# Kernel tuning notes

Measured on AMD Instinct MI355X. Metric: run time of the kernel, lower is better.

Reference implementation:

```python
import jax, jax.numpy as jnp
import numpy as np

M, N, D = 512, 4096, 128
H = N // D  # 32
L = 4096   # cache length


def setup_inputs() -> dict:
    key = jax.random.key(0)
    ks = jax.random.split(key, 6)
    s = 1.0 / np.sqrt(N)
    return {
        "X": jax.random.normal(ks[0], (M, N), jnp.float32),
        "W_q": jax.random.normal(ks[1], (N, N), jnp.float32) * s,
        "W_k": jax.random.normal(ks[2], (N, N), jnp.float32) * s,
        "W_v": jax.random.normal(ks[3], (N, N), jnp.float32) * s,
        "cache_K": jax.random.normal(ks[4], (H, L, D), jnp.float32),
        "cache_V": jax.random.normal(ks[5], (H, L, D), jnp.float32),
        "P": 3584,
    }


def reference(X, W_q, W_k, W_v, cache_K, cache_V, P):
    # nn.Linear(N, N, bias=False): y = x @ W.T
    q = (X @ W_q.T).reshape(M, H, D).transpose(1, 0, 2)  # [H, M, D]
    k = (X @ W_k.T).reshape(M, H, D).transpose(1, 0, 2)  # [H, M, D]
    v = (X @ W_v.T).reshape(M, H, D).transpose(1, 0, 2)  # [H, M, D]
    # KV-cache write at position P (static slice under jit for fixed P)
    cK = jax.lax.dynamic_update_slice(cache_K, k, (0, P, 0))  # [H, L, D]
    cV = jax.lax.dynamic_update_slice(cache_V, v, (0, P, 0))
    # attention over the full cache, no 1/sqrt(D) scaling (faithful to source)
    scores = jnp.einsum("hmd,hld->hml", q, cK)   # [H, M, L]
    weights = jax.nn.softmax(scores, axis=-1)
    out = jnp.einsum("hml,hld->hmd", weights, cV)  # [H, M, D]
    return out.transpose(1, 0, 2).reshape(M, H * D)  # [M, N]
```

## Files before the change

kernel.cpp:

```cpp
#include <hip/hip_runtime.h>
#include <hip/hip_fp16.h>

typedef _Float16 f16x8 __attribute__((ext_vector_type(8)));
typedef float    f32x4 __attribute__((ext_vector_type(4)));

#define MFMA16(a,b,c) __builtin_amdgcn_mfma_f32_16x16x32_f16(a,b,c,0,0,0)

__device__ __forceinline__ void gload_lds16(const void* g, void* l) {
  __builtin_amdgcn_global_load_lds(
      (const __attribute__((address_space(1))) void*)g,
      (__attribute__((address_space(3))) void*)l, 16, 0, 0);
}

__global__ void cvt_f32_f16(const float* __restrict__ src,
                            _Float16* __restrict__ dst, int n8) {
  int i = blockIdx.x * blockDim.x + threadIdx.x;
  int stride = gridDim.x * blockDim.x;
  for (; i < n8; i += stride) {
    const float4* s = (const float4*)src + 2 * (size_t)i;
    float4 a = s[0], b = s[1];
    f16x8 o;
    o[0]=(_Float16)a.x; o[1]=(_Float16)a.y; o[2]=(_Float16)a.z; o[3]=(_Float16)a.w;
    o[4]=(_Float16)b.x; o[5]=(_Float16)b.y; o[6]=(_Float16)b.z; o[7]=(_Float16)b.w;
    ((f16x8*)dst)[i] = o;
  }
}

__global__ __launch_bounds__(256) void qkv_gemm_fused(
    const _Float16* __restrict__ X,
    const float* __restrict__ Wq,
    const float* __restrict__ Wk,
    const float* __restrict__ Wv,
    const float* __restrict__ cK,
    const float* __restrict__ cV,
    _Float16* __restrict__ Q16,
    _Float16* __restrict__ Kc,
    _Float16* __restrict__ Vt16,
    const int* __restrict__ Pp)
{
  __shared__ __align__(16) _Float16 As[128 * 64];
  __shared__ __align__(16) _Float16 Bs[64 * 64];
  const int bid = blockIdx.x;
  const int tid = threadIdx.x;

  if (bid < 768) {
    const int xcd = bid & 7, s = bid >> 3;
    const int nt = xcd * 24 + (s >> 2);
    const int mt = s & 3;
    const int m0 = mt * 128, n0 = nt * 64;
    const int wave = tid >> 6, lane = tid & 63;
    const int g = lane >> 4, c = lane & 15;
    const int wr = wave >> 1, wc = wave & 1;
    const float* Wp = (n0 < 4096) ? Wq : ((n0 < 8192) ? Wk : Wv);
    const int n0l = n0 & 4095;
    const int ar  = lane >> 3;
    const int acs = (lane & 7) * 16;
    const int brow = tid >> 2;
    const int bc32 = (tid & 3) * 16;
    const float* wsrc = Wp + (size_t)(n0l + brow) * 4096 + bc32;
    const int bsw = (brow & 7) << 4;
    float4 breg[4];
#pragma unroll
    for (int i = 0; i < 4; i++) breg[i] = *(const float4*)(wsrc + i * 4);

    f32x4 acc[4][2] = {};
    for (int k0 = 0; k0 < 4096; k0 += 64) {
      __syncthreads();
#pragma unroll
      for (int p = 0; p < 4; p++) {
        int chunk = wave * 4 + p;
        int row = chunk * 8 + ar;
        gload_lds16((const char*)(X + (size_t)(m0 + row) * 4096 + k0) + (acs ^ ((row & 7) << 4)),
                    (char*)As + chunk * 1024);
      }
      {
        const float* bv = (const float*)breg;
        f16x8 h0, h1;
#pragma unroll
        for (int i = 0; i < 8; i++) { h0[i] = (_Float16)bv[i]; h1[i] = (_Float16)bv[8 + i]; }
        char* rb = (char*)Bs + brow * 128;
        *(f16x8*)(rb + (((tid & 3) * 32)      ^ bsw)) = h0;
        *(f16x8*)(rb + (((tid & 3) * 32 + 16) ^ bsw)) = h1;
        if (k0 + 64 < 4096) {
          const float* ns = wsrc + k0 + 64;
#pragma unroll
          for (int i = 0; i < 4; i++) breg[i] = *(const float4*)(ns + i * 4);
        }
      }
      __syncthreads();
      f16x8 af[2][4], bf[2][2];
#pragma unroll
      for (int mi = 0; mi < 4; mi++) {
        int row = wr * 64 + mi * 16 + c;
        int sw = (row & 7) << 4;
#pragma unroll
        for (int kc = 0; kc < 2; kc++)
          af[kc][mi] = *(const f16x8*)((const char*)As + row * 128 + ((kc * 64 + g * 16) ^ sw));
      }
#pragma unroll
      for (int ni = 0; ni < 2; ni++) {
        int row = wc * 32 + ni * 16 + c;
        int sw = (row & 7) << 4;
#pragma unroll
        for (int kc = 0; kc < 2; kc++)
          bf[kc][ni] = *(const f16x8*)((const char*)Bs + row * 128 + ((kc * 64 + g * 16) ^ sw));
      }
#pragma unroll
      for (int kc = 0; kc < 2; kc++)
#pragma unroll
        for (int mi = 0; mi < 4; mi++)
#pragma unroll
          for (int ni = 0; ni < 2; ni++)
            acc[mi][ni] = MFMA16(af[kc][mi], bf[kc][ni], acc[mi][ni]);
    }
    const int p = Pp[0];
    const int wsel = n0 >> 12;
    const int h = (n0 & 4095) >> 7;
    const int dbase = n0 & 127;
#pragma unroll
    for (int mi = 0; mi < 4; mi++) {
#pragma unroll
      for (int ni = 0; ni < 2; ni++) {
#pragma unroll
        for (int j = 0; j < 4; j++) {
          int m = m0 + wr * 64 + mi * 16 + 4 * g + j;
          int d = dbase + wc * 32 + ni * 16 + c;
          _Float16 hv = (_Float16)acc[mi][ni][j];
          if (wsel == 0)      Q16[(size_t)(h * 512 + m) * 128 + d] = hv;
          else if (wsel == 1) Kc[(size_t)(h * 4096 + p + m) * 128 + d] = hv;
          else                Vt16[((size_t)h * 128 + d) * 4096 + p + m] = hv;
        }
      }
    }
    return;
  }

  const int p = Pp[0];
  const int cb = bid - 768;
  if (cb < 512) {
    const int total = 32 * 4096 * 16;
    const int stride = 512 * 256;
    for (int i = cb * 256 + tid; i < total; i += stride) {
      int l = (i >> 4) & 4095;
      if ((unsigned)(l - p) < 512u) continue;
      const float4* s = (const float4*)cK + 2 * (size_t)i;
      float4 a = s[0], b = s[1];
      f16x8 o;
      o[0]=(_Float16)a.x; o[1]=(_Float16)a.y; o[2]=(_Float16)a.z; o[3]=(_Float16)a.w;
      o[4]=(_Float16)b.x; o[5]=(_Float16)b.y; o[6]=(_Float16)b.z; o[7]=(_Float16)b.w;
      ((f16x8*)Kc)[i] = o;
    }
  } else {
    _Float16 (*t)[72] = (_Float16 (*)[72])As;
    const int r = tid >> 4, c4 = (tid & 15) * 4;
    const int d = tid >> 2, lc = (tid & 3) * 16;
#pragma unroll
    for (int rep = 0; rep < 2; rep++) {
      int b = (cb - 512) * 2 + rep;
      int h = b >> 7, rest = b & 127;
      int lt = rest >> 1, dt = rest & 1;
      int l0 = lt * 64, d0 = dt * 64;
      __syncthreads();
#pragma unroll
      for (int i = 0; i < 4; i++) {
        int l = r + i * 16;
        float4 v = *(const float4*)&cV[((size_t)h * 4096 + l0 + l) * 128 + d0 + c4];
        t[c4 + 0][l] = (_Float16)v.x;
        t[c4 + 1][l] = (_Float16)v.y;
        t[c4 + 2][l] = (_Float16)v.z;
        t[c4 + 3][l] = (_Float16)v.w;
      }
      __syncthreads();
#pragma unroll
      for (int i = 0; i < 2; i++) {
        int l = l0 + lc + i * 8;
        if ((unsigned)(l - p) < 512u) continue;
        f16x8 o = *(const f16x8*)&t[d][lc + i * 8];
        *(f16x8*)&Vt16[((size_t)h * 128 + d0 + d) * 4096 + l] = o;
      }
    }
  }
}

__global__ __launch_bounds__(512, 2) void attn_part(
    const _Float16* __restrict__ Q16,
    const _Float16* __restrict__ Kc,
    const _Float16* __restrict__ Vt,
    float* __restrict__ Opart,
    float* __restrict__ Mpart,
    float* __restrict__ Lpart)
{
  __shared__ __align__(16) _Float16 Ks[64 * 128];
  __shared__ __align__(16) _Float16 Vs[128 * 64];
  __shared__ __align__(16) _Float16 Pl[8][16][68];
  const int bid = blockIdx.x;
  const int xcd = bid & 7, s = bid >> 3;
  const int group = xcd * 16 + (s >> 2);
  const int mt = s & 3;
  const int ls = group >> 5, h = group & 31;
  const int m0 = mt * 128;
  const int tid = threadIdx.x, wave = tid >> 6, lane = tid & 63;
  const int g = lane >> 4, c = lane & 15;
  const int mw = m0 + wave * 16;
  const _Float16* Kh  = Kc + (size_t)h * 4096 * 128;
  const _Float16* Vth = Vt + (size_t)h * 128 * 4096;
  f16x8 qf[4];
#pragma unroll
  for (int kc = 0; kc < 4; kc++)
    qf[kc] = *(const f16x8*)&Q16[(size_t)(h * 512 + mw + c) * 128 + kc * 32 + g * 8];
  f32x4 o[8] = {};
  float mrow[4] = {-3e38f, -3e38f, -3e38f, -3e38f};
  float lrow[4] = {0.f, 0.f, 0.f, 0.f};
  const int klr = lane >> 4, klb = (lane & 15) * 16;
  const int vlr = lane >> 3, vlb = (lane & 7) * 16;

  const int l_begin = ls * 1024;
  for (int l0 = l_begin; l0 < l_begin + 1024; l0 += 64) {
    __syncthreads();
#pragma unroll
    for (int p = 0; p < 2; p++) {
      int chunk = p * 8 + wave;
      int kr = chunk * 4 + klr;
      gload_lds16((const char*)Kh + (size_t)(l0 + kr) * 256 + (klb ^ ((kr & 7) << 4)),
                  (char*)Ks + chunk * 1024);
      int vd = chunk * 8 + vlr;
      gload_lds16((const char*)Vth + (size_t)vd * 8192 + (size_t)l0 * 2 + (vlb ^ ((vd & 7) << 4)),
                  (char*)Vs + chunk * 1024);
    }
    __syncthreads();
    f32x4 sc[4] = {};
#pragma unroll
    for (int ni = 0; ni < 4; ni++) {
      int kr = ni * 16 + c;
      f16x8 kf[4];
#pragma unroll
      for (int kc = 0; kc < 4; kc++)
        kf[kc] = *(const f16x8*)((const char*)Ks + kr * 256 + ((kc * 64 + g * 16) ^ ((kr & 7) << 4)));
#pragma unroll
      for (int kc = 0; kc < 4; kc++)
        sc[ni] = MFMA16(qf[kc], kf[kc], sc[ni]);
    }
    float scale[4];
#pragma unroll
    for (int j = 0; j < 4; j++) {
      float tm = sc[0][j];
#pragma unroll
      for (int ni = 1; ni < 4; ni++) tm = fmaxf(tm, sc[ni][j]);
      tm = fmaxf(tm, __shfl_xor(tm, 1, 64));
      tm = fmaxf(tm, __shfl_xor(tm, 2, 64));
      tm = fmaxf(tm, __shfl_xor(tm, 4, 64));
      tm = fmaxf(tm, __shfl_xor(tm, 8, 64));
      float mn = fmaxf(mrow[j], tm);
      scale[j] = __expf(mrow[j] - mn);
      mrow[j] = mn;
    }
    float rs[4] = {0.f, 0.f, 0.f, 0.f};
#pragma unroll
    for (int ni = 0; ni < 4; ni++) {
#pragma unroll
      for (int j = 0; j < 4; j++) {
        float pv = __expf(sc[ni][j] - mrow[j]);
        sc[ni][j] = pv;
        rs[j] += pv;
      }
    }
#pragma unroll
    for (int j = 0; j < 4; j++) {
      rs[j] += __shfl_xor(rs[j], 1, 64);
      rs[j] += __shfl_xor(rs[j], 2, 64);
      rs[j] += __shfl_xor(rs[j], 4, 64);
      rs[j] += __shfl_xor(rs[j], 8, 64);
      lrow[j] = lrow[j] * scale[j] + rs[j];
    }
#pragma unroll
    for (int dn = 0; dn < 8; dn++)
#pragma unroll
      for (int j = 0; j < 4; j++) o[dn][j] *= scale[j];
#pragma unroll
    for (int ni = 0; ni < 4; ni++)
#pragma unroll
      for (int j = 0; j < 4; j++)
        Pl[wave][4 * g + j][ni * 16 + c] = (_Float16)sc[ni][j];
    f16x8 pa[2];
#pragma unroll
    for (int kc = 0; kc < 2; kc++)
      pa[kc] = *(const f16x8*)&Pl[wave][c][kc * 32 + g * 8];
#pragma unroll
    for (int dn = 0; dn < 8; dn++) {
      int vr = dn * 16 + c;
#pragma unroll
      for (int kc = 0; kc < 2; kc++) {
        f16x8 vb = *(const f16x8*)((const char*)Vs + vr * 128 + ((kc * 64 + g * 16) ^ ((vr & 7) << 4)));
        o[dn] = MFMA16(pa[kc], vb, o[dn]);
      }
    }
  }
  const size_t pbase = ((size_t)(ls * 32 + h) * 512);
#pragma unroll
  for (int dn = 0; dn < 8; dn++) {
#pragma unroll
    for (int j = 0; j < 4; j++) {
      int m = mw + 4 * g + j;
      Opart[(pbase + m) * 128 + dn * 16 + c] = o[dn][j];
    }
  }
  if (c == 0) {
#pragma unroll
    for (int j = 0; j < 4; j++) {
      int m = mw + 4 * g + j;
      Mpart[pbase + m] = mrow[j];
      Lpart[pbase + m] = lrow[j];
    }
  }
}

__global__ __launch_bounds__(256) void attn_combine(
    const float* __restrict__ Opart,
    const float* __restrict__ Mpart,
    const float* __restrict__ Lpart,
    float* __restrict__ out)
{
  int idx = blockIdx.x * 256 + threadIdx.x;
  int row = idx >> 5;
  int d4  = idx & 31;
  int h = row >> 9, m = row & 511;
  float Ms[4];
  float mx = -3e38f;
#pragma unroll
  for (int s = 0; s < 4; s++) {
    Ms[s] = Mpart[(size_t)(s * 32 + h) * 512 + m];
    mx = fmaxf(mx, Ms[s]);
  }
  float lsum = 0.f;
  float4 acc = make_float4(0.f, 0.f, 0.f, 0.f);
#pragma unroll
  for (int s = 0; s < 4; s++) {
    float w = __expf(Ms[s] - mx);
    lsum += w * Lpart[(size_t)(s * 32 + h) * 512 + m];
    float4 ov = ((const float4*)(Opart + ((size_t)(s * 32 + h) * 512 + m) * 128))[d4];
    acc.x += w * ov.x; acc.y += w * ov.y; acc.z += w * ov.z; acc.w += w * ov.w;
  }
  float inv = 1.f / lsum;
  float4 r = make_float4(acc.x * inv, acc.y * inv, acc.z * inv, acc.w * inv);
  *(float4*)&out[(size_t)m * 4096 + h * 128 + d4 * 4] = r;
}

extern "C" void kernel_launch(void* const* d_in, const int* in_sizes, int n_in,
                              void* d_out, int out_size, void* d_ws, size_t ws_size,
                              hipStream_t stream) {
  const float* X  = (const float*)d_in[0];
  const float* Wq = (const float*)d_in[1];
  const float* Wk = (const float*)d_in[2];
  const float* Wv = (const float*)d_in[3];
  const float* cK = (const float*)d_in[4];
  const float* cV = (const float*)d_in[5];
  const int*   Pp = (const int*)d_in[6];
  float* out = (float*)d_out;

  char* ws = (char*)d_ws;
  _Float16* X16  = (_Float16*)(ws);
  float* Opart = (float*)(ws + ((size_t)4  << 20));
  float* Mpart = (float*)(ws + ((size_t)36 << 20));
  float* Lpart = (float*)(ws + ((size_t)37 << 20));
  _Float16* Q16  = (_Float16*)(ws + ((size_t)100 << 20));
  _Float16* K16  = (_Float16*)(ws + ((size_t)104 << 20));
  _Float16* V16t = (_Float16*)(ws + ((size_t)136 << 20));

  cvt_f32_f16<<<dim3(1024), dim3(256), 0, stream>>>(X, X16, 512 * 4096 / 8);

  qkv_gemm_fused<<<dim3(768 + 512 + 2048), dim3(256), 0, stream>>>(
      X16, Wq, Wk, Wv, cK, cV, Q16, K16, V16t, Pp);

  attn_part<<<dim3(512), dim3(512), 0, stream>>>(Q16, K16, V16t, Opart, Mpart, Lpart);
  attn_combine<<<dim3(2048), dim3(256), 0, stream>>>(Opart, Mpart, Lpart, out);
}
```

Measured before the change: 224.3 us.

## Fuse fp32 KV-cache conversion into attention tile loads, drop fp16 cache pre-pass

Removes the separate cache-conversion and V-transpose blocks from the QKV GEMM launch. The attention kernel now reads the fp32 cache directly, converts and transposes it in registers, and writes it to LDS with register prefetch of the next tile. It only uses the fp16 K/V buffers for tiles inside the freshly written window. This avoids writing and re-reading a full fp16 copy of the cache. In exchange it drops the async global-to-LDS loads, raises register pressure, and changes occupancy to 4 blocks, while partial outputs are stored as fp16 to halve combine traffic at some precision cost.

```diff
diff --git a/kernel.cpp b/kernel.cpp
--- a/kernel.cpp
+++ b/kernel.cpp
@@ -2,6 +2,7 @@
 #include <hip/hip_fp16.h>
 
 typedef _Float16 f16x8 __attribute__((ext_vector_type(8)));
+typedef _Float16 f16x4 __attribute__((ext_vector_type(4)));
 typedef float    f32x4 __attribute__((ext_vector_type(4)));
 
 #define MFMA16(a,b,c) __builtin_amdgcn_mfma_f32_16x16x32_f16(a,b,c,0,0,0)
@@ -26,13 +27,11 @@
   }
 }
 
-__global__ __launch_bounds__(256) void qkv_gemm_fused(
+__global__ __launch_bounds__(256) void qkv_gemm(
     const _Float16* __restrict__ X,
     const float* __restrict__ Wq,
     const float* __restrict__ Wk,
     const float* __restrict__ Wv,
-    const float* __restrict__ cK,
-    const float* __restrict__ cV,
     _Float16* __restrict__ Q16,
     _Float16* __restrict__ Kc,
     _Float16* __restrict__ Vt16,
@@ -41,154 +40,106 @@
   __shared__ __align__(16) _Float16 As[128 * 64];
   __shared__ __align__(16) _Float16 Bs[64 * 64];
   const int bid = blockIdx.x;
-  const int tid = threadIdx.x;
-
-  if (bid < 768) {
-    const int xcd = bid & 7, s = bid >> 3;
-    const int nt = xcd * 24 + (s >> 2);
-    const int mt = s & 3;
-    const int m0 = mt * 128, n0 = nt * 64;
-    const int wave = tid >> 6, lane = tid & 63;
-    const int g = lane >> 4, c = lane & 15;
-    const int wr = wave >> 1, wc = wave & 1;
-    const float* Wp = (n0 < 4096) ? Wq : ((n0 < 8192) ? Wk : Wv);
-    const int n0l = n0 & 4095;
-    const int ar  = lane >> 3;
-    const int acs = (lane & 7) * 16;
-    const int brow = tid >> 2;
-    const int bc32 = (tid & 3) * 16;
-    const float* wsrc = Wp + (size_t)(n0l + brow) * 4096 + bc32;
-    const int bsw = (brow & 7) << 4;
-    float4 breg[4];
-#pragma unroll
-    for (int i = 0; i < 4; i++) breg[i] = *(const float4*)(wsrc + i * 4);
-
-    f32x4 acc[4][2] = {};
-    for (int k0 = 0; k0 < 4096; k0 += 64) {
-      __syncthreads();
-#pragma unroll
-      for (int p = 0; p < 4; p++) {
-        int chunk = wave * 4 + p;
-        int row = chunk * 8 + ar;
-        gload_lds16((const char*)(X + (size_t)(m0 + row) * 4096 + k0) + (acs ^ ((row & 7) << 4)),
-                    (char*)As + chunk * 1024);
-      }
-      {
-        const float* bv = (const float*)breg;
-        f16x8 h0, h1;
-#pragma unroll
-        for (int i = 0; i < 8; i++) { h0[i] = (_Float16)bv[i]; h1[i] = (_Float16)bv[8 + i]; }
-        char* rb = (char*)Bs + brow * 128;
-        *(f16x8*)(rb + (((tid & 3) * 32)      ^ bsw)) = h0;
-        *(f16x8*)(rb + (((tid & 3) * 32 + 16) ^ bsw)) = h1;
-        if (k0 + 64 < 4096) {
-          const float* ns = wsrc + k0 + 64;
-#pragma unroll
-          for (int i = 0; i < 4; i++) breg[i] = *(const float4*)(ns + i * 4);
-        }
-      }
-      __syncthreads();
-      f16x8 af[2][4], bf[2][2];
-#pragma unroll
-      for (int mi = 0; mi < 4; mi++) {
-        int row = wr * 64 + mi * 16 + c;
-        int sw = (row & 7) << 4;
-#pragma unroll
-        for (int kc = 0; kc < 2; kc++)
-          af[kc][mi] = *(const f16x8*)((const char*)As + row * 128 + ((kc * 64 + g * 16) ^ sw));
-      }
-#pragma unroll
-      for (int ni = 0; ni < 2; ni++) {
-        int row = wc * 32 + ni * 16 + c;
-        int sw = (row & 7) << 4;
-#pragma unroll
-        for (int kc = 0; kc < 2; kc++)
-          bf[kc][ni] = *(const f16x8*)((const char*)Bs + row * 128 + ((kc * 64 + g * 16) ^ sw));
-      }
+  const int xcd = bid & 7, s = bid >> 3;
+  const int nt = xcd * 24 + (s >> 2);
+  const int mt = s & 3;
+  const int m0 = mt * 128, n0 = nt * 64;
+  const int tid = threadIdx.x, wave = tid >> 6, lane = tid & 63;
+  const int g = lane >> 4, c = lane & 15;
+  const int wr = wave >> 1, wc = wave & 1;
+  const float* Wp = (n0 < 4096) ? Wq : ((n0 < 8192) ? Wk : Wv);
+  const int n0l = n0 & 4095;
+  const int ar  = lane >> 3;
+  const int acs = (lane & 7) * 16;
+  const int brow = tid >> 2;
+  const int bc32 = (tid & 3) * 16;
+  const float* wsrc = Wp + (size_t)(n0l + brow) * 4096 + bc32;
+  const int bsw = (brow & 7) << 4;
+  float4 breg[4];
+#pragma unroll
+  for (int i = 0; i < 4; i++) breg[i] = *(const float4*)(wsrc + i * 4);
+
+  f32x4 acc[4][2] = {};
+  for (int k0 = 0; k0 < 4096; k0 += 64) {
+    __syncthreads();
+#pragma unroll
+    for (int p = 0; p < 4; p++) {
+      int chunk = wave * 4 + p;
+      int row = chunk * 8 + ar;
+      gload_lds16((const char*)(X + (size_t)(m0 + row) * 4096 + k0) + (acs ^ ((row & 7) << 4)),
+                  (char*)As + chunk * 1024);
+    }
+    {
+      const float* bv = (const float*)breg;
+      f16x8 h0, h1;
+#pragma unroll
+      for (int i = 0; i < 8; i++) { h0[i] = (_Float16)bv[i]; h1[i] = (_Float16)bv[8 + i]; }
+      char* rb = (char*)Bs + brow * 128;
+      *(f16x8*)(rb + (((tid & 3) * 32)      ^ bsw)) = h0;
+      *(f16x8*)(rb + (((tid & 3) * 32 + 16) ^ bsw)) = h1;
+      if (k0 + 64 < 4096) {
+        const float* ns = wsrc + k0 + 64;
+#pragma unroll
+        for (int i = 0; i < 4; i++) breg[i] = *(const float4*)(ns + i * 4);
+      }
+    }
+    __syncthreads();
+    f16x8 af[2][4], bf[2][2];
+#pragma unroll
+    for (int mi = 0; mi < 4; mi++) {
+      int row = wr * 64 + mi * 16 + c;
+      int sw = (row & 7) << 4;
 #pragma unroll
       for (int kc = 0; kc < 2; kc++)
-#pragma unroll
-        for (int mi = 0; mi < 4; mi++)
-#pragma unroll
-          for (int ni = 0; ni < 2; ni++)
-            acc[mi][ni] = MFMA16(af[kc][mi], bf[kc][ni], acc[mi][ni]);
-    }
-    const int p = Pp[0];
-    const int wsel = n0 >> 12;
-    const int h = (n0 & 4095) >> 7;
-    const int dbase = n0 & 127;
-#pragma unroll
-    for (int mi = 0; mi < 4; mi++) {
-#pragma unroll
-      for (int ni = 0; ni < 2; ni++) {
-#pragma unroll
-        for (int j = 0; j < 4; j++) {
-          int m = m0 + wr * 64 + mi * 16 + 4 * g + j;
-          int d = dbase + wc * 32 + ni * 16 + c;
-          _Float16 hv = (_Float16)acc[mi][ni][j];
-          if (wsel == 0)      Q16[(size_t)(h * 512 + m) * 128 + d] = hv;
-          else if (wsel == 1) Kc[(size_t)(h * 4096 + p + m) * 128 + d] = hv;
-          else                Vt16[((size_t)h * 128 + d) * 4096 + p + m] = hv;
-        }
-      }
-    }
-    return;
-  }
-
+        af[kc][mi] = *(const f16x8*)((const char*)As + row * 128 + ((kc * 64 + g * 16) ^ sw));
+    }
+#pragma unroll
+    for (int ni = 0; ni < 2; ni++) {
+      int row = wc * 32 + ni * 16 + c;
+      int sw = (row & 7) << 4;
+#pragma unroll
+      for (int kc = 0; kc < 2; kc++)
+        bf[kc][ni] = *(const f16x8*)((const char*)Bs + row * 128 + ((kc * 64 + g * 16) ^ sw));
+    }
+#pragma unroll
+    for (int kc = 0; kc < 2; kc++)
+#pragma unroll
+      for (int mi = 0; mi < 4; mi++)
+#pragma unroll
+        for (int ni = 0; ni < 2; ni++)
+          acc[mi][ni] = MFMA16(af[kc][mi], bf[kc][ni], acc[mi][ni]);
+  }
   const int p = Pp[0];
-  const int cb = bid - 768;
-  if (cb < 512) {
-    const int total = 32 * 4096 * 16;
-    const int stride = 512 * 256;
-    for (int i = cb * 256 + tid; i < total; i += stride) {
-      int l = (i >> 4) & 4095;
-      if ((unsigned)(l - p) < 512u) continue;
-      const float4* s = (const float4*)cK + 2 * (size_t)i;
-      float4 a = s[0], b = s[1];
-      f16x8 o;
-      o[0]=(_Float16)a.x; o[1]=(_Float16)a.y; o[2]=(_Float16)a.z; o[3]=(_Float16)a.w;
-      o[4]=(_Float16)b.x; o[5]=(_Float16)b.y; o[6]=(_Float16)b.z; o[7]=(_Float16)b.w;
-      ((f16x8*)Kc)[i] = o;
-    }
-  } else {
-    _Float16 (*t)[72] = (_Float16 (*)[72])As;
-    const int r = tid >> 4, c4 = (tid & 15) * 4;
-    const int d = tid >> 2, lc = (tid & 3) * 16;
-#pragma unroll
-    for (int rep = 0; rep < 2; rep++) {
-      int b = (cb - 512) * 2 + rep;
-      int h = b >> 7, rest = b & 127;
-      int lt = rest >> 1, dt = rest & 1;
-      int l0 = lt * 64, d0 = dt * 64;
-      __syncthreads();
-#pragma unroll
-      for (int i = 0; i < 4; i++) {
-        int l = r + i * 16;
-        float4 v = *(const float4*)&cV[((size_t)h * 4096 + l0 + l) * 128 + d0 + c4];
-        t[c4 + 0][l] = (_Float16)v.x;
-        t[c4 + 1][l] = (_Float16)v.y;
-        t[c4 + 2][l] = (_Float16)v.z;
-        t[c4 + 3][l] = (_Float16)v.w;
-      }
-      __syncthreads();
-#pragma unroll
-      for (int i = 0; i < 2; i++) {
-        int l = l0 + lc + i * 8;
-        if ((unsigned)(l - p) < 512u) continue;
-        f16x8 o = *(const f16x8*)&t[d][lc + i * 8];
-        *(f16x8*)&Vt16[((size_t)h * 128 + d0 + d) * 4096 + l] = o;
-      }
-    }
-  }
-}
-
-__global__ __launch_bounds__(512, 2) void attn_part(
+  const int wsel = n0 >> 12;
+  const int h = (n0 & 4095) >> 7;
+  const int dbase = n0 & 127;
+#pragma unroll
+  for (int mi = 0; mi < 4; mi++) {
+#pragma unroll
+    for (int ni = 0; ni < 2; ni++) {
+#pragma unroll
+      for (int j = 0; j < 4; j++) {
+        int m = m0 + wr * 64 + mi * 16 + 4 * g + j;
+        int d = dbase + wc * 32 + ni * 16 + c;
+        _Float16 hv = (_Float16)acc[mi][ni][j];
+        if (wsel == 0)      Q16[(size_t)(h * 512 + m) * 128 + d] = hv;
+        else if (wsel == 1) Kc[(size_t)(h * 4096 + p + m) * 128 + d] = hv;
+        else                Vt16[((size_t)h * 128 + d) * 4096 + p + m] = hv;
+      }
+    }
+  }
+}
+
+__global__ __launch_bounds__(512, 4) void attn_part(
     const _Float16* __restrict__ Q16,
-    const _Float16* __restrict__ Kc,
+    const _Float16* __restrict__ K16,
     const _Float16* __restrict__ Vt,
-    float* __restrict__ Opart,
+    const float* __restrict__ cK,
+    const float* __restrict__ cV,
+    _Float16* __restrict__ Opart,
     float* __restrict__ Mpart,
-    float* __restrict__ Lpart)
+    float* __restrict__ Lpart,
+    const int* __restrict__ Pp)
 {
   __shared__ __align__(16) _Float16 Ks[64 * 128];
   __shared__ __align__(16) _Float16 Vs[128 * 64];
@@ -202,8 +153,11 @@
   const int tid = threadIdx.x, wave = tid >> 6, lane = tid & 63;
   const int g = lane >> 4, c = lane & 15;
   const int mw = m0 + wave * 16;
-  const _Float16* Kh  = Kc + (size_t)h * 4096 * 128;
-  const _Float16* Vth = Vt + (size_t)h * 128 * 4096;
+  const int p = Pp[0];
+  const _Float16* K16h = K16 + (size_t)h * 4096 * 128;
+  const _Float16* Vth  = Vt  + (size_t)h * 128 * 4096;
+  const float* cKh = cK + (size_t)h * 4096 * 128;
+  const float* cVh = cV + (size_t)h * 4096 * 128;
   f16x8 qf[4];
 #pragma unroll
   for (int kc = 0; kc < 4; kc++)
@@ -211,31 +165,80 @@
   f32x4 o[8] = {};
   float mrow[4] = {-3e38f, -3e38f, -3e38f, -3e38f};
   float lrow[4] = {0.f, 0.f, 0.f, 0.f};
-  const int klr = lane >> 4, klb = (lane & 15) * 16;
-  const int vlr = lane >> 3, vlb = (lane & 7) * 16;
+
+  const int kr = tid >> 3, kq = tid & 7;
+  const int ksw = (kr & 7) << 4;
+  const int dp = (tid & 63) * 2, lg = tid >> 6;
+  float4 ka4[4];
+  float4 va4[4];
+  bool cur16 = false;
+
+  auto loadTile = [&](int l0) {
+    bool is16 = ((unsigned)(l0 - p) < 512u);
+    cur16 = is16;
+    if (!is16) {
+      const float* ks = cKh + (size_t)(l0 + kr) * 128 + kq * 16;
+#pragma unroll
+      for (int i = 0; i < 4; i++) ka4[i] = ((const float4*)ks)[i];
+      const float* vs0 = cVh + (size_t)(l0 + lg * 8) * 128 + dp;
+#pragma unroll
+      for (int i = 0; i < 4; i++) {
+        float2 a = *(const float2*)(vs0 + (size_t)(2 * i) * 128);
+        float2 b = *(const float2*)(vs0 + (size_t)(2 * i + 1) * 128);
+        va4[i] = make_float4(a.x, a.y, b.x, b.y);
+      }
+    } else {
+      const _Float16* ks = K16h + (size_t)(l0 + kr) * 128 + kq * 16;
+      ka4[0] = *(const float4*)(ks);
+      ka4[1] = *(const float4*)(ks + 8);
+      const _Float16* vs0 = Vth + (size_t)dp * 4096 + l0 + lg * 8;
+      va4[0] = *(const float4*)(vs0);
+      va4[1] = *(const float4*)(vs0 + 4096);
+    }
+  };
+  auto writeTile = [&]() {
+    f16x8 h0, h1;
+    if (!cur16) {
+      h0[0]=(_Float16)ka4[0].x; h0[1]=(_Float16)ka4[0].y; h0[2]=(_Float16)ka4[0].z; h0[3]=(_Float16)ka4[0].w;
+      h0[4]=(_Float16)ka4[1].x; h0[5]=(_Float16)ka4[1].y; h0[6]=(_Float16)ka4[1].z; h0[7]=(_Float16)ka4[1].w;
+      h1[0]=(_Float16)ka4[2].x; h1[1]=(_Float16)ka4[2].y; h1[2]=(_Float16)ka4[2].z; h1[3]=(_Float16)ka4[2].w;
+      h1[4]=(_Float16)ka4[3].x; h1[5]=(_Float16)ka4[3].y; h1[6]=(_Float16)ka4[3].z; h1[7]=(_Float16)ka4[3].w;
+    } else {
+      h0 = *(f16x8*)&ka4[0];
+      h1 = *(f16x8*)&ka4[1];
+    }
+    char* rb = (char*)Ks + kr * 256;
+    *(f16x8*)(rb + ((kq * 32)      ^ ksw)) = h0;
+    *(f16x8*)(rb + ((kq * 32 + 16) ^ ksw)) = h1;
+    f16x8 v0, v1;
+    if (!cur16) {
+      v0[0]=(_Float16)va4[0].x; v0[1]=(_Float16)va4[0].z; v0[2]=(_Float16)va4[1].x; v0[3]=(_Float16)va4[1].z;
+      v0[4]=(_Float16)va4[2].x; v0[5]=(_Float16)va4[2].z; v0[6]=(_Float16)va4[3].x; v0[7]=(_Float16)va4[3].z;
+      v1[0]=(_Float16)va4[0].y; v1[1]=(_Float16)va4[0].w; v1[2]=(_Float16)va4[1].y; v1[3]=(_Float16)va4[1].w;
+      v1[4]=(_Float16)va4[2].y; v1[5]=(_Float16)va4[2].w; v1[6]=(_Float16)va4[3].y; v1[7]=(_Float16)va4[3].w;
+    } else {
+      v0 = *(f16x8*)&va4[0];
+      v1 = *(f16x8*)&va4[1];
+    }
+    *(f16x8*)((char*)Vs + (size_t)dp * 128       + ((lg * 16) ^ ((dp & 7) << 4)))       = v0;
+    *(f16x8*)((char*)Vs + (size_t)(dp + 1) * 128 + ((lg * 16) ^ (((dp + 1) & 7) << 4))) = v1;
+  };
 
   const int l_begin = ls * 1024;
+  loadTile(l_begin);
   for (int l0 = l_begin; l0 < l_begin + 1024; l0 += 64) {
     __syncthreads();
-#pragma unroll
-    for (int p = 0; p < 2; p++) {
-      int chunk = p * 8 + wave;
-      int kr = chunk * 4 + klr;
-      gload_lds16((const char*)Kh + (size_t)(l0 + kr) * 256 + (klb ^ ((kr & 7) << 4)),
-                  (char*)Ks + chunk * 1024);
-      int vd = chunk * 8 + vlr;
-      gload_lds16((const char*)Vth + (size_t)vd * 8192 + (size_t)l0 * 2 + (vlb ^ ((vd & 7) << 4)),
-                  (char*)Vs + chunk * 1024);
-    }
+    writeTile();
+    if (l0 + 64 < l_begin + 1024) loadTile(l0 + 64);
     __syncthreads();
     f32x4 sc[4] = {};
 #pragma unroll
     for (int ni = 0; ni < 4; ni++) {
-      int kr = ni * 16 + c;
+      int krr = ni * 16 + c;
       f16x8 kf[4];
 #pragma unroll
       for (int kc = 0; kc < 4; kc++)
-        kf[kc] = *(const f16x8*)((const char*)Ks + kr * 256 + ((kc * 64 + g * 16) ^ ((kr & 7) << 4)));
+        kf[kc] = *(const f16x8*)((const char*)Ks + krr * 256 + ((kc * 64 + g * 16) ^ ((krr & 7) << 4)));
 #pragma unroll
       for (int kc = 0; kc < 4; kc++)
         sc[ni] = MFMA16(qf[kc], kf[kc], sc[ni]);
@@ -301,7 +304,7 @@
 #pragma unroll
     for (int j = 0; j < 4; j++) {
       int m = mw + 4 * g + j;
-      Opart[(pbase + m) * 128 + dn * 16 + c] = o[dn][j];
+      Opart[(pbase + m) * 128 + dn * 16 + c] = (_Float16)o[dn][j];
     }
   }
   if (c == 0) {
@@ -315,7 +318,7 @@
 }
 
 __global__ __launch_bounds__(256) void attn_combine(
-    const float* __restrict__ Opart,
+    const _Float16* __restrict__ Opart,
     const float* __restrict__ Mpart,
     const float* __restrict__ Lpart,
     float* __restrict__ out)
@@ -337,8 +340,9 @@
   for (int s = 0; s < 4; s++) {
     float w = __expf(Ms[s] - mx);
     lsum += w * Lpart[(size_t)(s * 32 + h) * 512 + m];
-    float4 ov = ((const float4*)(Opart + ((size_t)(s * 32 + h) * 512 + m) * 128))[d4];
-    acc.x += w * ov.x; acc.y += w * ov.y; acc.z += w * ov.z; acc.w += w * ov.w;
+    f16x4 ov = *(const f16x4*)(Opart + ((size_t)(s * 32 + h) * 512 + m) * 128 + d4 * 4);
+    acc.x += w * (float)ov[0]; acc.y += w * (float)ov[1];
+    acc.z += w * (float)ov[2]; acc.w += w * (float)ov[3];
   }
   float inv = 1.f / lsum;
   float4 r = make_float4(acc.x * inv, acc.y * inv, acc.z * inv, acc.w * inv);
@@ -359,7 +363,7 @@
 
   char* ws = (char*)d_ws;
   _Float16* X16  = (_Float16*)(ws);
-  float* Opart = (float*)(ws + ((size_t)4  << 20));
+  _Float16* Opart = (_Float16*)(ws + ((size_t)4  << 20));
   float* Mpart = (float*)(ws + ((size_t)36 << 20));
   float* Lpart = (float*)(ws + ((size_t)37 << 20));
   _Float16* Q16  = (_Float16*)(ws + ((size_t)100 << 20));
@@ -367,10 +371,8 @@
   _Float16* V16t = (_Float16*)(ws + ((size_t)136 << 20));
 
   cvt_f32_f16<<<dim3(1024), dim3(256), 0, stream>>>(X, X16, 512 * 4096 / 8);
-
-  qkv_gemm_fused<<<dim3(768 + 512 + 2048), dim3(256), 0, stream>>>(
-      X16, Wq, Wk, Wv, cK, cV, Q16, K16, V16t, Pp);
-
-  attn_part<<<dim3(512), dim3(512), 0, stream>>>(Q16, K16, V16t, Opart, Mpart, Lpart);
+  qkv_gemm<<<dim3(768), dim3(256), 0, stream>>>(X16, Wq, Wk, Wv, Q16, K16, V16t, Pp);
+  attn_part<<<dim3(512), dim3(512), 0, stream>>>(Q16, K16, V16t, cK, cV,
+                                                 Opart, Mpart, Lpart, Pp);
   attn_combine<<<dim3(2048), dim3(256), 0, stream>>>(Opart, Mpart, Lpart, out);
 }
```

Result: no change. 227.6 us (+1.5%).
